# Optimization experiments

Measured on AMD Instinct MI355X. Metric: run time of the kernel, lower is better.

Reference implementation:

```python
import math
import jax, jax.numpy as jnp
import numpy as np

IMAGE_SIZE = (256, 704)
N_VOX = (200, 200, 4)
VOX_SIZE = (0.5, 0.5, 1.5)
BN_EPS = 1e-5


def _voxel_points_homog():
    # matches get_points: meshgrid(indexing='ij') * voxel_size + origin, origin = [0,0,-1] - n_vox/2*vox
    nx, ny, nz = N_VOX
    idx = jnp.stack(jnp.meshgrid(jnp.arange(nx), jnp.arange(ny), jnp.arange(nz), indexing='ij')).astype(jnp.float32)  # [3,nx,ny,nz]
    vs = jnp.array(VOX_SIZE, jnp.float32)
    origin = jnp.array([0.0, 0.0, -1.0], jnp.float32) - jnp.array(N_VOX, jnp.float32) / 2.0 * vs
    pts = idx * vs.reshape(3, 1, 1, 1) + origin.reshape(3, 1, 1, 1)
    P = nx * ny * nz
    pts = pts.reshape(3, P)
    return jnp.concatenate([pts, jnp.ones((1, P), jnp.float32)], axis=0)  # [4,P]


def _backproject(feat, proj, aug_t, stride):
    # feat: [N,C,H,W]; proj: [N,3,4]; aug_t: [N,2] (u,v translation from img_aug_matrix[:, :2, -1])
    N, C, H, W = feat.shape
    homog = _voxel_points_homog()            # [4,P]
    P = homog.shape[1]
    p2i = jnp.einsum('nij,jp->nip', proj, homog)  # [N,3,P]
    Z = p2i[:, 2]
    Zs = jnp.where(jnp.abs(Z) > 1e-6, Z, 1e-6)    # guard div-by-0; such points are invalid anyway
    u = p2i[:, 0] / Zs + aug_t[:, 0:1]
    v = p2i[:, 1] / Zs + aug_t[:, 1:2]
    u_fm = jnp.round(u / stride).astype(jnp.int32)
    v_fm = jnp.round(v / stride).astype(jnp.int32)
    valid = (u_fm >= 0) & (v_fm >= 0) & (u_fm < W) & (v_fm < H) & (Z > 0)  # [N,P]
    sel = (N - 1) - jnp.argmax(valid[::-1], axis=0)   # [P]
    any_valid = valid.any(axis=0)                     # [P]
    ar = jnp.arange(P)
    u_s = jnp.clip(u_fm[sel, ar], 0, W - 1)
    v_s = jnp.clip(v_fm[sel, ar], 0, H - 1)
    g = feat[sel, :, v_s, u_s]                        # [P,C] single fused gather
    vol = (g * any_valid[:, None].astype(feat.dtype)).T  # [C,P]
    return vol.reshape(C, *N_VOX)


def _forward(mlvl_feats, points, lidar2image, img_aug_matrix, lidar_aug_matrix,
             conv_w, conv_b, bn_gamma, bn_beta, bn_mean, bn_var):
    stride = float(math.ceil(IMAGE_SIZE[1] / mlvl_feats.shape[-1]))  # static

    def per_batch(feat, iam, lam, l2i):
        iam_r = iam.at[..., -1].set(0.0)                 # zero last column
        proj = (iam_r @ l2i @ lam[None])[:, :3, :]       # [N,3,4]
        aug_t = iam[:, 0:2, -1]                          # [N,2]
        return _backproject(feat, proj, aug_t, stride)

    vols = jax.vmap(per_batch)(mlvl_feats, img_aug_matrix, lidar_aug_matrix, lidar2image)  # [B,C,nx,ny,nz]
    w = jnp.transpose(points, (0, 2, 3, 1))[:, None]     # [B,1,nx,ny,nz]
    bev = (vols * w).sum(axis=-1)                        # [B,C,nx,ny]  (cat of single z-slice)
    y = jnp.einsum('bchw,oc->bohw', bev, conv_w) + conv_b[None, :, None, None]
    inv = jax.lax.rsqrt(bn_var + BN_EPS)
    y = (y - bn_mean[None, :, None, None]) * (inv * bn_gamma)[None, :, None, None] + bn_beta[None, :, None, None]
    return jax.nn.relu(y)


def setup_inputs() -> dict:
    key = jax.random.key(0)
    ks = jax.random.split(key, 12)
    B, N, C, H, W = 1, 6, 256, 32, 88
    return {
        'mlvl_feats': jax.random.normal(ks[0], (B, N, C, H, W), jnp.float32),
        'points': jax.random.uniform(ks[1], (B, N_VOX[2], N_VOX[0], N_VOX[1]), jnp.float32),
        'ori_points': 0,
        'img': 0,
        'lidar2camera': jax.random.normal(ks[2], (B, N, 4, 4), jnp.float32),
        'lidar2image': jax.random.normal(ks[3], (B, N, 4, 4), jnp.float32),
        'cam_intrinsic': jax.random.normal(ks[4], (B, N, 4, 4), jnp.float32),
        'cam_2_lidar': jax.random.normal(ks[5], (B, N, 4, 4), jnp.float32),
        'img_aug_matrix': jnp.eye(4, dtype=jnp.float32)[None, None] + 0.1 * jax.random.normal(ks[6], (B, N, 4, 4), jnp.float32),
        'lidar_aug_matrix': jnp.eye(4, dtype=jnp.float32)[None] + 0.1 * jax.random.normal(ks[7], (B, 4, 4), jnp.float32),
        'img_metas': 0,
        'conv_w': 0.02 * jax.random.normal(ks[8], (80, 256), jnp.float32),
        'conv_b': jax.random.normal(ks[9], (80,), jnp.float32) * 0.01,
        'bn_gamma': jnp.ones((80,), jnp.float32),
        'bn_beta': jnp.zeros((80,), jnp.float32),
        'bn_mean': jnp.zeros((80,), jnp.float32),
        'bn_var': jnp.ones((80,), jnp.float32),
    }


def reference(mlvl_feats, points, ori_points, img, lidar2camera, lidar2image,
              cam_intrinsic, cam_2_lidar, img_aug_matrix, lidar_aug_matrix,
              img_metas, conv_w, conv_b, bn_gamma, bn_beta, bn_mean, bn_var):
    return _forward(mlvl_feats, points, lidar2image, img_aug_matrix, lidar_aug_matrix,
                    conv_w, conv_b, bn_gamma, bn_beta, bn_mean, bn_var)
```

## Files before the change

### kernel.cpp

```cpp
#include <hip/hip_runtime.h>
#include <math.h>

typedef __attribute__((ext_vector_type(8))) short bf16x8;
typedef __attribute__((ext_vector_type(4))) float f32x4;

#define N_CAM 6
#define C_IN 256
#define C_OUT 80
#define FH 32
#define FW 88
#define NXG 200
#define NYG 200
#define S_SPATIAL (NXG*NYG)
#define POS_PER_CAM (FH*FW)
#define NPOS (N_CAM*POS_PER_CAM)

#define WS_PA     0
#define WS_BIAS   128
#define WS_WF     256
#define WS_FEAT2B 10496

__device__ __forceinline__ unsigned short f2bf(float f) {
    unsigned u = __builtin_bit_cast(unsigned, f);
    u += 0x7fffu + ((u >> 16) & 1u);
    return (unsigned short)(u >> 16);
}
__device__ __forceinline__ float bf2f(unsigned short u) {
    return __builtin_bit_cast(float, ((unsigned)u) << 16);
}

__global__ __launch_bounds__(128) void k_prep(const float* __restrict__ iam,
                       const float* __restrict__ lam,
                       const float* __restrict__ l2i,
                       const float* __restrict__ conv_w, const float* __restrict__ conv_b,
                       const float* __restrict__ gamma, const float* __restrict__ beta,
                       const float* __restrict__ mean, const float* __restrict__ var,
                       float* __restrict__ pa, uint4* __restrict__ wf,
                       float* __restrict__ bias2) {
    int bid = blockIdx.x;
    int t = threadIdx.x;
    if (bid == 0) {
        if (t < N_CAM) {
            int n = t;
            const float* A = iam + n * 16;
            const float* L = l2i + n * 16;
            float M1[12];
            #pragma unroll
            for (int i = 0; i < 3; ++i)
                #pragma unroll
                for (int j = 0; j < 4; ++j) {
                    float acc = __fmul_rn(A[i*4+0], L[0*4+j]);
                    acc = __fmaf_rn(A[i*4+1], L[1*4+j], acc);
                    acc = __fmaf_rn(A[i*4+2], L[2*4+j], acc);
                    M1[i*4+j] = acc;
                }
            #pragma unroll
            for (int i = 0; i < 3; ++i)
                #pragma unroll
                for (int j = 0; j < 4; ++j) {
                    float acc = __fmul_rn(M1[i*4+0], lam[0*4+j]);
                    acc = __fmaf_rn(M1[i*4+1], lam[1*4+j], acc);
                    acc = __fmaf_rn(M1[i*4+2], lam[2*4+j], acc);
                    acc = __fmaf_rn(M1[i*4+3], lam[3*4+j], acc);
                    pa[n*12 + i*4 + j] = acc;
                }
            pa[72 + n*2 + 0] = A[0*4 + 3];
            pa[72 + n*2 + 1] = A[1*4 + 3];
        } else if (t >= 48) {
            int o = t - 48;
            float inv = 1.0f / sqrtf(var[o] + 1e-5f);
            float sc = __fmul_rn(inv, gamma[o]);
            bias2[o] = __fadd_rn(__fmul_rn(__fsub_rn(conv_b[o], mean[o]), sc), beta[o]);
        }
        return;
    }
    if (t >= 64) return;
    int fi = bid - 1;
    int nt = fi >> 3, ks = fi & 7;
    int o  = nt * 16 + (t & 15);
    int cb = ks * 32 + (t >> 4) * 8;
    float inv = 1.0f / sqrtf(var[o] + 1e-5f);
    float sc = __fmul_rn(inv, gamma[o]);
    unsigned short e[8];
    #pragma unroll
    for (int j = 0; j < 8; ++j)
        e[j] = f2bf(__fmul_rn(conv_w[o * C_IN + cb + j], sc));
    uint4 u;
    u.x = e[0] | ((unsigned)e[1] << 16);
    u.y = e[2] | ((unsigned)e[3] << 16);
    u.z = e[4] | ((unsigned)e[5] << 16);
    u.w = e[6] | ((unsigned)e[7] << 16);
    wf[fi * 64 + t] = u;
}

__global__ __launch_bounds__(256) void k_fconv(const float* __restrict__ feat,
                                               const bf16x8* __restrict__ wf,
                                               unsigned short* __restrict__ feat2b) {
    __shared__ uint4 sfo[2048];
    int b = blockIdx.x, t = threadIdx.x;
    int n = b / 44, p0 = (b % 44) * 64;
    const float* fn = feat + (size_t)n * C_IN * POS_PER_CAM + p0;
    uint2* sfo2 = reinterpret_cast<uint2*>(sfo);
    #pragma unroll
    for (int i = 0; i < 16; ++i) {
        int task = i * 256 + t;
        int pl = task & 63, cg = task >> 6;
        int c0 = cg * 4;
        float v0 = fn[(c0+0) * POS_PER_CAM + pl];
        float v1 = fn[(c0+1) * POS_PER_CAM + pl];
        float v2 = fn[(c0+2) * POS_PER_CAM + pl];
        float v3 = fn[(c0+3) * POS_PER_CAM + pl];
        unsigned lo = f2bf(v0) | ((unsigned)f2bf(v1) << 16);
        unsigned hi = f2bf(v2) | ((unsigned)f2bf(v3) << 16);
        int ksp = c0 >> 5;
        int q   = (c0 & 31) >> 3;
        int lf  = (pl & 15) + (q << 4);
        int f   = ((pl >> 4) * 8 + ksp) * 64 + lf;
        sfo2[f * 2 + (cg & 1)] = make_uint2(lo, hi);
    }
    __syncthreads();

    int wv = t >> 6, l = t & 63;
    const bf16x8* sfrag = reinterpret_cast<const bf16x8*>(sfo);
    bf16x8 a[8];
    #pragma unroll
    for (int ks = 0; ks < 8; ++ks)
        a[ks] = sfrag[(wv * 8 + ks) * 64 + l];
    int posb = b * 64 + wv * 16 + ((l >> 4) << 2);
    #pragma unroll
    for (int nt = 0; nt < 5; ++nt) {
        f32x4 acc = {0.f, 0.f, 0.f, 0.f};
        #pragma unroll
        for (int ks = 0; ks < 8; ++ks) {
            bf16x8 bb = wf[(nt * 8 + ks) * 64 + l];
            acc = __builtin_amdgcn_mfma_f32_16x16x32_bf16(a[ks], bb, acc, 0, 0, 0);
        }
        #pragma unroll
        for (int r = 0; r < 4; ++r)
            feat2b[(size_t)(posb + r) * C_OUT + nt * 16 + (l & 15)] = f2bf(acc[r]);
    }
}

__global__ __launch_bounds__(256) void k_main(const unsigned short* __restrict__ feat2b,
                                              const float* __restrict__ pa_g,
                                              const float* __restrict__ bias_g,
                                              const float* __restrict__ points,
                                              float* __restrict__ out) {
    __shared__ float s_pa[84];
    __shared__ float s_bias[C_OUT];
    __shared__ int   s_base[256];
    __shared__ float s_w[256];
    __shared__ float s_y[64 * 81];
    int t = threadIdx.x;
    int col0 = blockIdx.x * 64;

    if (t < 84) s_pa[t] = pa_g[t];
    else if (t >= 128 && t < 128 + C_OUT) s_bias[t - 128] = bias_g[t - 128];
    __syncthreads();

    {
        int cl = t & 63, z = t >> 6;
        int col = col0 + cl;
        int ix = col / NYG, iy = col % NYG;
        float x  = (float)ix * 0.5f - 50.0f;
        float y  = (float)iy * 0.5f - 50.0f;
        float zc = (float)z  * 1.5f - 4.0f;
        int sel_base = 0;
        bool any = false;
        #pragma unroll
        for (int n = 0; n < N_CAM; ++n) {
            const float* P = s_pa + n * 12;
            float px = __fadd_rn(__fadd_rn(__fadd_rn(__fmul_rn(P[0], x), __fmul_rn(P[1], y)), __fmul_rn(P[2], zc)), P[3]);
            float py = __fadd_rn(__fadd_rn(__fadd_rn(__fmul_rn(P[4], x), __fmul_rn(P[5], y)), __fmul_rn(P[6], zc)), P[7]);
            float pz = __fadd_rn(__fadd_rn(__fadd_rn(__fmul_rn(P[8], x), __fmul_rn(P[9], y)), __fmul_rn(P[10], zc)), P[11]);
            float Z = pz;
            float Zs = (fabsf(Z) > 1e-6f) ? Z : 1e-6f;
            float u = __fadd_rn(px / Zs, s_pa[72 + n*2 + 0]);
            float v = __fadd_rn(py / Zs, s_pa[72 + n*2 + 1]);
            float uf = rintf(__fmul_rn(u, 0.125f));
            float vf = rintf(__fmul_rn(v, 0.125f));
            int ui = (int)uf, vi = (int)vf;
            bool val = (ui >= 0) & (vi >= 0) & (ui < FW) & (vi < FH) & (Z > 0.0f);
            if (val) { sel_base = ((n * FH + vi) * FW + ui) * C_OUT; any = true; }
        }
        float w = 0.0f;
        if (any) w = points[z * S_SPATIAL + col];
        else sel_base = 0;
        s_base[z * 64 + cl] = sel_base;
        s_w[z * 64 + cl] = w;
    }
    __syncthreads();

    #pragma unroll
    for (int it = 0; it < 20; ++it) {
        int idx = it * 256 + t;
        int c = idx / 80, o = idx - c * 80;
        float acc =            __fmul_rn(s_w[0*64+c], bf2f(feat2b[s_base[0*64+c] + o]));
        acc = __fadd_rn(acc, __fmul_rn(s_w[1*64+c], bf2f(feat2b[s_base[1*64+c] + o])));
        acc = __fadd_rn(acc, __fmul_rn(s_w[2*64+c], bf2f(feat2b[s_base[2*64+c] + o])));
        acc = __fadd_rn(acc, __fmul_rn(s_w[3*64+c], bf2f(feat2b[s_base[3*64+c] + o])));
        float yv = fmaxf(__fadd_rn(acc, s_bias[o]), 0.0f);
        s_y[c * 81 + o] = yv;
    }
    __syncthreads();

    #pragma unroll
    for (int it = 0; it < 20; ++it) {
        int idx = it * 256 + t;
        int o = idx >> 6, c = idx & 63;
        out[o * S_SPATIAL + col0 + c] = s_y[c * 81 + o];
    }
}

extern "C" void kernel_launch(void* const* d_in, const int* in_sizes, int n_in,
                              void* d_out, int out_size, void* d_ws, size_t ws_size,
                              hipStream_t stream) {
    const float* feat   = (const float*)d_in[0];
    const float* points = (const float*)d_in[1];
    const float* l2i    = (const float*)d_in[5];
    const float* iam    = (const float*)d_in[8];
    const float* lam    = (const float*)d_in[9];
    const float* conv_w = (const float*)d_in[11];
    const float* conv_b = (const float*)d_in[12];
    const float* gamma  = (const float*)d_in[13];
    const float* beta   = (const float*)d_in[14];
    const float* mean   = (const float*)d_in[15];
    const float* var    = (const float*)d_in[16];

    float* ws     = (float*)d_ws;
    float* pa     = ws + WS_PA;
    float* bias2  = ws + WS_BIAS;
    uint4* wf     = (uint4*)(ws + WS_WF);
    unsigned short* feat2b = (unsigned short*)(ws + WS_FEAT2B);
    float* out    = (float*)d_out;

    hipLaunchKernelGGL(k_prep, dim3(41), dim3(128), 0, stream,
                       iam, lam, l2i, conv_w, conv_b, gamma, beta, mean, var,
                       pa, wf, bias2);
    hipLaunchKernelGGL(k_fconv, dim3(NPOS / 64), dim3(256), 0, stream,
                       feat, (const bf16x8*)wf, feat2b);
    hipLaunchKernelGGL(k_main, dim3(S_SPATIAL / 64), dim3(256), 0, stream,
                       feat2b, pa, bias2, points, out);
}
```

Baseline: 25.12 us.

## Fold prep kernel into fconv and main, vectorize gather loads

Removes the separate prep kernel. Each fconv block now builds the BN-scaled bf16 weight fragments itself in shared memory, and each main block recomputes the projection matrices and fused bias locally. This saves one launch and the serialization between kernels. fconv blocks shrink to 32 positions and 128 threads, which doubles the grid. The main gather now uses 16-byte loads covering 8 channels per thread instead of scalar bf16 loads. In exchange, every block redundantly repeats the weight conversion work (about 20 KB read per fconv block) and the matrix setup.

```diff
diff --git a/kernel.cpp b/kernel.cpp
--- a/kernel.cpp
+++ b/kernel.cpp
@@ -14,11 +14,7 @@
 #define S_SPATIAL (NXG*NYG)
 #define POS_PER_CAM (FH*FW)
 #define NPOS (N_CAM*POS_PER_CAM)
-
-#define WS_PA     0
-#define WS_BIAS   128
-#define WS_WF     256
-#define WS_FEAT2B 10496
+#define TPOS 32
 
 __device__ __forceinline__ unsigned short f2bf(float f) {
     unsigned u = __builtin_bit_cast(unsigned, f);
@@ -29,82 +25,22 @@
     return __builtin_bit_cast(float, ((unsigned)u) << 16);
 }
 
-__global__ __launch_bounds__(128) void k_prep(const float* __restrict__ iam,
-                       const float* __restrict__ lam,
-                       const float* __restrict__ l2i,
-                       const float* __restrict__ conv_w, const float* __restrict__ conv_b,
-                       const float* __restrict__ gamma, const float* __restrict__ beta,
-                       const float* __restrict__ mean, const float* __restrict__ var,
-                       float* __restrict__ pa, uint4* __restrict__ wf,
-                       float* __restrict__ bias2) {
-    int bid = blockIdx.x;
-    int t = threadIdx.x;
-    if (bid == 0) {
-        if (t < N_CAM) {
-            int n = t;
-            const float* A = iam + n * 16;
-            const float* L = l2i + n * 16;
-            float M1[12];
-            #pragma unroll
-            for (int i = 0; i < 3; ++i)
-                #pragma unroll
-                for (int j = 0; j < 4; ++j) {
-                    float acc = __fmul_rn(A[i*4+0], L[0*4+j]);
-                    acc = __fmaf_rn(A[i*4+1], L[1*4+j], acc);
-                    acc = __fmaf_rn(A[i*4+2], L[2*4+j], acc);
-                    M1[i*4+j] = acc;
-                }
-            #pragma unroll
-            for (int i = 0; i < 3; ++i)
-                #pragma unroll
-                for (int j = 0; j < 4; ++j) {
-                    float acc = __fmul_rn(M1[i*4+0], lam[0*4+j]);
-                    acc = __fmaf_rn(M1[i*4+1], lam[1*4+j], acc);
-                    acc = __fmaf_rn(M1[i*4+2], lam[2*4+j], acc);
-                    acc = __fmaf_rn(M1[i*4+3], lam[3*4+j], acc);
-                    pa[n*12 + i*4 + j] = acc;
-                }
-            pa[72 + n*2 + 0] = A[0*4 + 3];
-            pa[72 + n*2 + 1] = A[1*4 + 3];
-        } else if (t >= 48) {
-            int o = t - 48;
-            float inv = 1.0f / sqrtf(var[o] + 1e-5f);
-            float sc = __fmul_rn(inv, gamma[o]);
-            bias2[o] = __fadd_rn(__fmul_rn(__fsub_rn(conv_b[o], mean[o]), sc), beta[o]);
-        }
-        return;
-    }
-    if (t >= 64) return;
-    int fi = bid - 1;
-    int nt = fi >> 3, ks = fi & 7;
-    int o  = nt * 16 + (t & 15);
-    int cb = ks * 32 + (t >> 4) * 8;
-    float inv = 1.0f / sqrtf(var[o] + 1e-5f);
-    float sc = __fmul_rn(inv, gamma[o]);
-    unsigned short e[8];
-    #pragma unroll
-    for (int j = 0; j < 8; ++j)
-        e[j] = f2bf(__fmul_rn(conv_w[o * C_IN + cb + j], sc));
-    uint4 u;
-    u.x = e[0] | ((unsigned)e[1] << 16);
-    u.y = e[2] | ((unsigned)e[3] << 16);
-    u.z = e[4] | ((unsigned)e[5] << 16);
-    u.w = e[6] | ((unsigned)e[7] << 16);
-    wf[fi * 64 + t] = u;
-}
-
-__global__ __launch_bounds__(256) void k_fconv(const float* __restrict__ feat,
-                                               const bf16x8* __restrict__ wf,
+__global__ __launch_bounds__(128) void k_fconv(const float* __restrict__ feat,
+                                               const float* __restrict__ conv_w,
+                                               const float* __restrict__ gamma,
+                                               const float* __restrict__ var,
                                                unsigned short* __restrict__ feat2b) {
-    __shared__ uint4 sfo[2048];
+    __shared__ uint4 sfo[1024];
+    __shared__ uint4 wfrag[2560];
     int b = blockIdx.x, t = threadIdx.x;
-    int n = b / 44, p0 = (b % 44) * 64;
+    int n = b / 88, p0 = (b % 88) * TPOS;
     const float* fn = feat + (size_t)n * C_IN * POS_PER_CAM + p0;
     uint2* sfo2 = reinterpret_cast<uint2*>(sfo);
+
     #pragma unroll
     for (int i = 0; i < 16; ++i) {
-        int task = i * 256 + t;
-        int pl = task & 63, cg = task >> 6;
+        int task = i * 128 + t;
+        int pl = task & 31, cg = task >> 5;
         int c0 = cg * 4;
         float v0 = fn[(c0+0) * POS_PER_CAM + pl];
         float v1 = fn[(c0+1) * POS_PER_CAM + pl];
@@ -118,21 +54,43 @@
         int f   = ((pl >> 4) * 8 + ksp) * 64 + lf;
         sfo2[f * 2 + (cg & 1)] = make_uint2(lo, hi);
     }
+    #pragma unroll
+    for (int i = 0; i < 20; ++i) {
+        int task = i * 128 + t;
+        int fi = task >> 6, l = task & 63;
+        int nt = fi >> 3, ks = fi & 7;
+        int o  = nt * 16 + (l & 15);
+        int cb = ks * 32 + (l >> 4) * 8;
+        float inv = 1.0f / sqrtf(var[o] + 1e-5f);
+        float sc = __fmul_rn(inv, gamma[o]);
+        const float* wrow = conv_w + o * C_IN + cb;
+        unsigned short e[8];
+        #pragma unroll
+        for (int j = 0; j < 8; ++j)
+            e[j] = f2bf(__fmul_rn(wrow[j], sc));
+        uint4 u;
+        u.x = e[0] | ((unsigned)e[1] << 16);
+        u.y = e[2] | ((unsigned)e[3] << 16);
+        u.z = e[4] | ((unsigned)e[5] << 16);
+        u.w = e[6] | ((unsigned)e[7] << 16);
+        wfrag[task] = u;
+    }
     __syncthreads();
 
     int wv = t >> 6, l = t & 63;
     const bf16x8* sfrag = reinterpret_cast<const bf16x8*>(sfo);
+    const bf16x8* wfr   = reinterpret_cast<const bf16x8*>(wfrag);
     bf16x8 a[8];
     #pragma unroll
     for (int ks = 0; ks < 8; ++ks)
         a[ks] = sfrag[(wv * 8 + ks) * 64 + l];
-    int posb = b * 64 + wv * 16 + ((l >> 4) << 2);
+    int posb = b * TPOS + wv * 16 + ((l >> 4) << 2);
     #pragma unroll
     for (int nt = 0; nt < 5; ++nt) {
         f32x4 acc = {0.f, 0.f, 0.f, 0.f};
         #pragma unroll
         for (int ks = 0; ks < 8; ++ks) {
-            bf16x8 bb = wf[(nt * 8 + ks) * 64 + l];
+            bf16x8 bb = wfr[(nt * 8 + ks) * 64 + l];
             acc = __builtin_amdgcn_mfma_f32_16x16x32_bf16(a[ks], bb, acc, 0, 0, 0);
         }
         #pragma unroll
@@ -142,8 +100,14 @@
 }
 
 __global__ __launch_bounds__(256) void k_main(const unsigned short* __restrict__ feat2b,
-                                              const float* __restrict__ pa_g,
-                                              const float* __restrict__ bias_g,
+                                              const float* __restrict__ iam,
+                                              const float* __restrict__ lam,
+                                              const float* __restrict__ l2i,
+                                              const float* __restrict__ conv_b,
+                                              const float* __restrict__ gamma,
+                                              const float* __restrict__ beta,
+                                              const float* __restrict__ mean,
+                                              const float* __restrict__ var,
                                               const float* __restrict__ points,
                                               float* __restrict__ out) {
     __shared__ float s_pa[84];
@@ -154,8 +118,38 @@
     int t = threadIdx.x;
     int col0 = blockIdx.x * 64;
 
-    if (t < 84) s_pa[t] = pa_g[t];
-    else if (t >= 128 && t < 128 + C_OUT) s_bias[t - 128] = bias_g[t - 128];
+    if (t < N_CAM) {
+        int n = t;
+        const float* A = iam + n * 16;
+        const float* L = l2i + n * 16;
+        float M1[12];
+        #pragma unroll
+        for (int i = 0; i < 3; ++i)
+            #pragma unroll
+            for (int j = 0; j < 4; ++j) {
+                float acc = __fmul_rn(A[i*4+0], L[0*4+j]);
+                acc = __fmaf_rn(A[i*4+1], L[1*4+j], acc);
+                acc = __fmaf_rn(A[i*4+2], L[2*4+j], acc);
+                M1[i*4+j] = acc;
+            }
+        #pragma unroll
+        for (int i = 0; i < 3; ++i)
+            #pragma unroll
+            for (int j = 0; j < 4; ++j) {
+                float acc = __fmul_rn(M1[i*4+0], lam[0*4+j]);
+                acc = __fmaf_rn(M1[i*4+1], lam[1*4+j], acc);
+                acc = __fmaf_rn(M1[i*4+2], lam[2*4+j], acc);
+                acc = __fmaf_rn(M1[i*4+3], lam[3*4+j], acc);
+                s_pa[n*12 + i*4 + j] = acc;
+            }
+        s_pa[72 + n*2 + 0] = A[0*4 + 3];
+        s_pa[72 + n*2 + 1] = A[1*4 + 3];
+    } else if (t >= 64 && t < 64 + C_OUT) {
+        int o = t - 64;
+        float inv = 1.0f / sqrtf(var[o] + 1e-5f);
+        float sc = __fmul_rn(inv, gamma[o]);
+        s_bias[o] = __fadd_rn(__fmul_rn(__fsub_rn(conv_b[o], mean[o]), sc), beta[o]);
+    }
     __syncthreads();
 
     {
@@ -192,15 +186,34 @@
     __syncthreads();
 
     #pragma unroll
-    for (int it = 0; it < 20; ++it) {
-        int idx = it * 256 + t;
-        int c = idx / 80, o = idx - c * 80;
-        float acc =            __fmul_rn(s_w[0*64+c], bf2f(feat2b[s_base[0*64+c] + o]));
-        acc = __fadd_rn(acc, __fmul_rn(s_w[1*64+c], bf2f(feat2b[s_base[1*64+c] + o])));
-        acc = __fadd_rn(acc, __fmul_rn(s_w[2*64+c], bf2f(feat2b[s_base[2*64+c] + o])));
-        acc = __fadd_rn(acc, __fmul_rn(s_w[3*64+c], bf2f(feat2b[s_base[3*64+c] + o])));
-        float yv = fmaxf(__fadd_rn(acc, s_bias[o]), 0.0f);
-        s_y[c * 81 + o] = yv;
+    for (int it = 0; it < 3; ++it) {
+        int task = it * 256 + t;
+        if (task < 640) {
+            int c = task / 10, o8 = task - c * 10;
+            uint4 v0 = reinterpret_cast<const uint4*>(feat2b + s_base[0*64 + c])[o8];
+            uint4 v1 = reinterpret_cast<const uint4*>(feat2b + s_base[1*64 + c])[o8];
+            uint4 v2 = reinterpret_cast<const uint4*>(feat2b + s_base[2*64 + c])[o8];
+            uint4 v3 = reinterpret_cast<const uint4*>(feat2b + s_base[3*64 + c])[o8];
+            float w0 = s_w[0*64 + c], w1 = s_w[1*64 + c];
+            float w2 = s_w[2*64 + c], w3 = s_w[3*64 + c];
+            #pragma unroll
+            for (int e = 0; e < 8; ++e) {
+                unsigned u0 = (&v0.x)[e >> 1], u1 = (&v1.x)[e >> 1];
+                unsigned u2 = (&v2.x)[e >> 1], u3 = (&v3.x)[e >> 1];
+                int sh = (e & 1) << 4;
+                float f0 = bf2f((unsigned short)(u0 >> sh));
+                float f1 = bf2f((unsigned short)(u1 >> sh));
+                float f2 = bf2f((unsigned short)(u2 >> sh));
+                float f3 = bf2f((unsigned short)(u3 >> sh));
+                float acc =            __fmul_rn(w0, f0);
+                acc = __fadd_rn(acc, __fmul_rn(w1, f1));
+                acc = __fadd_rn(acc, __fmul_rn(w2, f2));
+                acc = __fadd_rn(acc, __fmul_rn(w3, f3));
+                int o = o8 * 8 + e;
+                float yv = fmaxf(__fadd_rn(acc, s_bias[o]), 0.0f);
+                s_y[c * 81 + o] = yv;
+            }
+        }
     }
     __syncthreads();
 
@@ -227,18 +240,12 @@
     const float* mean   = (const float*)d_in[15];
     const float* var    = (const float*)d_in[16];
 
-    float* ws     = (float*)d_ws;
-    float* pa     = ws + WS_PA;
-    float* bias2  = ws + WS_BIAS;
-    uint4* wf     = (uint4*)(ws + WS_WF);
-    unsigned short* feat2b = (unsigned short*)(ws + WS_FEAT2B);
-    float* out    = (float*)d_out;
-
-    hipLaunchKernelGGL(k_prep, dim3(41), dim3(128), 0, stream,
-                       iam, lam, l2i, conv_w, conv_b, gamma, beta, mean, var,
-                       pa, wf, bias2);
-    hipLaunchKernelGGL(k_fconv, dim3(NPOS / 64), dim3(256), 0, stream,
-                       feat, (const bf16x8*)wf, feat2b);
+    unsigned short* feat2b = (unsigned short*)d_ws;
+    float* out = (float*)d_out;
+
+    hipLaunchKernelGGL(k_fconv, dim3(NPOS / TPOS), dim3(128), 0, stream,
+                       feat, conv_w, gamma, var, feat2b);
     hipLaunchKernelGGL(k_main, dim3(S_SPATIAL / 64), dim3(256), 0, stream,
-                       feat2b, pa, bias2, points, out);
-}
+                       feat2b, iam, lam, l2i, conv_b, gamma, beta, mean, var,
+                       points, out);
+}
```

Result: slower. 25.72 us (+2.4%).
